# Performance work log

Hardware: AMD Instinct MI355X
Metric: run time of the kernel (lower is better)

The kernel has to match this reference:

```python
import jax, jax.numpy as jnp
import numpy as np

N = 50000          # nodes
E = 600000         # edges
D_IN = 256         # input_feat_dim
H1 = 128           # hidden_dim1
H2 = 64            # hidden_dim2
DK = 64            # trs_depth (total key/value depth)
HEADS = 2


def setup_inputs() -> dict:
    key = jax.random.key(0)
    ks = jax.random.split(key, 12)
    inp = {
        "ns_emb": jax.random.normal(ks[0], (N, D_IN), dtype=jnp.float32),
        "edge_rows": jax.random.randint(ks[1], (E,), 0, N, dtype=jnp.int32),
        "edge_cols": jax.random.randint(ks[2], (E,), 0, N, dtype=jnp.int32),
        "edge_vals": jax.random.uniform(ks[3], (E,), dtype=jnp.float32),
        "condition": jax.random.normal(ks[4], (1, 128, H1), dtype=jnp.float32),
        # GCN linear weights (bias=False), stored [in, out]
        "W_hidden": jax.random.normal(ks[5], (D_IN, H1), dtype=jnp.float32) / np.sqrt(D_IN),
        "W_mu": jax.random.normal(ks[6], (H1, H2), dtype=jnp.float32) / np.sqrt(H1),
        "W_var": jax.random.normal(ks[7], (H1, H2), dtype=jnp.float32) / np.sqrt(H1),
        # MultiHeadAttention (bias-free) projections
        "Wq": jax.random.normal(ks[8], (H1, DK), dtype=jnp.float32) / np.sqrt(H1),
        "Wk": jax.random.normal(ks[9], (H1, DK), dtype=jnp.float32) / np.sqrt(H1),
        "Wv": jax.random.normal(ks[10], (H1, DK), dtype=jnp.float32) / np.sqrt(H1),
        "Wo": jax.random.normal(ks[11], (DK, H1), dtype=jnp.float32) / np.sqrt(DK),
    }
    return inp


def _spmm(rows, cols, vals, x):
    # sparse [N,N] @ x  via gather + segment-sum over COO edges
    gathered = vals[:, None] * x[cols]            # [E, d]
    return jax.ops.segment_sum(gathered, rows, num_segments=N)


def _gcn(x, W, rows, cols, vals):
    # dropout is identity in eval mode
    support = jax.nn.leaky_relu(x @ W)            # [N, out]
    out = _spmm(rows, cols, vals, support)        # [N, out]
    return jax.nn.leaky_relu(out)


def _mha(q, kv, Wq, Wk, Wv, Wo):
    # MoEL-style MultiHeadAttention, bias-free, no mask/dropout
    B, Lq, _ = q.shape
    Lk = kv.shape[1]
    dk = DK // HEADS
    Q = (q @ Wq).reshape(B, Lq, HEADS, dk).transpose(0, 2, 1, 3) * (dk ** -0.5)
    K = (kv @ Wk).reshape(B, Lk, HEADS, dk).transpose(0, 2, 1, 3)
    V = (kv @ Wv).reshape(B, Lk, HEADS, dk).transpose(0, 2, 1, 3)
    logits = jnp.einsum("bhqd,bhkd->bhqk", Q, K)
    w = jax.nn.softmax(logits, axis=-1)
    ctx = jnp.einsum("bhqk,bhkd->bhqd", w, V)
    ctx = ctx.transpose(0, 2, 1, 3).reshape(B, Lq, DK)
    return ctx @ Wo, w


def reference(ns_emb, edge_rows, edge_cols, edge_vals, condition,
              W_hidden, W_mu, W_var, Wq, Wk, Wv, Wo):
    hidden = _gcn(ns_emb, W_hidden, edge_rows, edge_cols, edge_vals)   # [N, H1]
    attended, _ = _mha(hidden[None], condition, Wq, Wk, Wv, Wo)        # [1, N, H1]
    h = attended[0]
    mu = _gcn(h, W_mu, edge_rows, edge_cols, edge_vals)                # [N, H2]
    var = _gcn(h, W_var, edge_rows, edge_cols, edge_vals)              # [N, H2]
    return mu, var
```

## Files before the change

### kernel.cpp

```cpp
#include <hip/hip_runtime.h>
#include <hip/hip_bf16.h>
#include <cstdint>


typedef __attribute__((ext_vector_type(8))) short short8;
typedef __attribute__((ext_vector_type(4))) float f32x4;
typedef __attribute__((ext_vector_type(4))) unsigned short ushort4_t;

__device__ __forceinline__ unsigned short f2bf(float f) {
    unsigned int u = __builtin_bit_cast(unsigned int, f);
    u += 0x7fffu + ((u >> 16) & 1u);
    return (unsigned short)(u >> 16);
}
__device__ __forceinline__ float bf2f(unsigned short v) {
    return __builtin_bit_cast(float, (unsigned int)v << 16);
}


__global__ void hist_kernel(const int* __restrict__ rows, int* __restrict__ cnt, int E) {
    int i = blockIdx.x * blockDim.x + threadIdx.x;
    if (i < E) atomicAdd(&cnt[rows[i]], 1);
}

__global__ void scan1_kernel(const int* __restrict__ cnt, int* __restrict__ excl,
                             int* __restrict__ bsum, int N) {
    __shared__ int sh[256];
    int t = threadIdx.x;
    int i = blockIdx.x * 256 + t;
    int v = (i < N) ? cnt[i] : 0;
    sh[t] = v;
    __syncthreads();
    for (int off = 1; off < 256; off <<= 1) {
        int x = (t >= off) ? sh[t - off] : 0;
        __syncthreads();
        sh[t] += x;
        __syncthreads();
    }
    if (i < N) excl[i] = sh[t] - v;
    if (t == 255) bsum[blockIdx.x] = sh[255];
}

__global__ void scan2_kernel(int* __restrict__ bsum, int nb) {
    __shared__ int sh[256];
    int t = threadIdx.x;
    int v = (t < nb) ? bsum[t] : 0;
    sh[t] = v;
    __syncthreads();
    for (int off = 1; off < 256; off <<= 1) {
        int x = (t >= off) ? sh[t - off] : 0;
        __syncthreads();
        sh[t] += x;
        __syncthreads();
    }
    if (t < nb) bsum[t] = sh[t] - v;
}

__global__ void scan3_kernel(const int* __restrict__ excl, const int* __restrict__ bsum,
                             int* __restrict__ row_start, int* __restrict__ cursor,
                             int N, int E) {
    int i = blockIdx.x * 256 + threadIdx.x;
    if (i < N) {
        int v = excl[i] + bsum[i >> 8];
        row_start[i] = v;
        cursor[i] = v;
    }
    if (i == 0) row_start[N] = E;
}

__global__ void scatter_kernel(const int* __restrict__ rows, const int* __restrict__ colsIn,
                               const float* __restrict__ valsIn, int* __restrict__ cursor,
                               int2* __restrict__ pack, int E) {
    int i = blockIdx.x * blockDim.x + threadIdx.x;
    if (i < E) {
        int r = rows[i];
        int p = atomicAdd(&cursor[r], 1);
        pack[p] = make_int2(colsIn[i], __float_as_int(valsIn[i]));
    }
}


__global__ __launch_bounds__(256) void prep_weights(
    const float* __restrict__ Wh, const float* __restrict__ Wq,
    const float* __restrict__ Wo, const float* __restrict__ Wmu,
    const float* __restrict__ Wvar,
    unsigned short* __restrict__ WhT, unsigned short* __restrict__ WqT,
    unsigned short* __restrict__ WoT, unsigned short* __restrict__ WmuT,
    unsigned short* __restrict__ WvarT)
{
    int idx = blockIdx.x * 256 + threadIdx.x;
    if (idx < 32768) {
        int n = idx & 127, k = idx >> 7;
        WhT[n * 256 + k] = f2bf(Wh[k * 128 + n]);
    } else if (idx < 40960) {
        int i = idx - 32768, n = i & 63, k = i >> 6;
        WqT[n * 128 + k] = f2bf(Wq[k * 64 + n]);
    } else if (idx < 49152) {
        int i = idx - 40960, n = i & 127, k = i >> 7;
        WoT[n * 64 + k] = f2bf(Wo[k * 128 + n]);
    } else if (idx < 57344) {
        int i = idx - 49152, n = i & 63, k = i >> 6;
        WmuT[n * 128 + k] = f2bf(Wmu[k * 64 + n]);
    } else if (idx < 65536) {
        int i = idx - 57344, n = i & 63, k = i >> 6;
        WvarT[n * 128 + k] = f2bf(Wvar[k * 64 + n]);
    }
}


__global__ __launch_bounds__(128) void kv_kernel(
    const float* __restrict__ cond, const float* __restrict__ Wk,
    const float* __restrict__ Wv, unsigned short* __restrict__ Ktt,
    unsigned short* __restrict__ Vt)
{
    int j = blockIdx.x;
    int t = threadIdx.x;
    __shared__ float c[128];
    c[t] = cond[j * 128 + t];
    __syncthreads();
    const float* W = (t < 64) ? Wk : Wv;
    int col = t & 63;
    float acc = 0.f;
#pragma unroll 8
    for (int k = 0; k < 128; ++k) acc = fmaf(c[k], W[k * 64 + col], acc);
    int h = col >> 5, d = col & 31;
    if (t < 64) Ktt[((size_t)h * 128 + j) * 32 + d] = f2bf(acc * 0.17677669529663687f);
    else        Vt[((size_t)h * 32 + d) * 128 + j] = f2bf(acc);
}


__global__ __launch_bounds__(256) void gcn1_gemm(
    const float* __restrict__ A, const unsigned short* __restrict__ BT,
    unsigned short* __restrict__ C, int M)
{
    __shared__ unsigned short As[128][72];
    __shared__ unsigned short Bs[128][72];

    const int tid = threadIdx.x;
    const int lane = tid & 63, wave = tid >> 6;
    const int wm = wave & 1, wn = wave >> 1;
    const int quad = lane >> 4, l16 = lane & 15;
    const int r0 = blockIdx.x * 128;

    f32x4 acc[4][4];
#pragma unroll
    for (int mt = 0; mt < 4; ++mt)
#pragma unroll
        for (int nt = 0; nt < 4; ++nt)
#pragma unroll
            for (int r = 0; r < 4; ++r) acc[mt][nt][r] = 0.f;

    for (int kc = 0; kc < 256; kc += 64) {
#pragma unroll
        for (int i = 0; i < 8; ++i) {
            int f = tid + 256 * i;
            int row = f >> 4, kq = (f & 15) << 2;
            int gr = r0 + row;
            if (gr >= M) gr = M - 1;
            float4 v = *reinterpret_cast<const float4*>(&A[(size_t)gr * 256 + kc + kq]);
            ushort4_t pv;
            pv[0] = f2bf(v.x); pv[1] = f2bf(v.y); pv[2] = f2bf(v.z); pv[3] = f2bf(v.w);
            *reinterpret_cast<ushort4_t*>(&As[row][kq]) = pv;
        }
#pragma unroll
        for (int i = 0; i < 4; ++i) {
            int f = tid + 256 * i;
            int n = f >> 3, k8 = (f & 7) << 3;
            *reinterpret_cast<short8*>(&Bs[n][k8]) =
                *reinterpret_cast<const short8*>(&BT[(size_t)n * 256 + kc + k8]);
        }
        __syncthreads();

#pragma unroll
        for (int ks = 0; ks < 2; ++ks) {
            const int koff = ks * 32 + quad * 8;
            short8 a[4], b[4];
#pragma unroll
            for (int mt = 0; mt < 4; ++mt)
                a[mt] = *reinterpret_cast<const short8*>(&As[wm * 64 + mt * 16 + l16][koff]);
#pragma unroll
            for (int nt = 0; nt < 4; ++nt)
                b[nt] = *reinterpret_cast<const short8*>(&Bs[wn * 64 + nt * 16 + l16][koff]);
#pragma unroll
            for (int mt = 0; mt < 4; ++mt)
#pragma unroll
                for (int nt = 0; nt < 4; ++nt)
                    acc[mt][nt] = __builtin_amdgcn_mfma_f32_16x16x32_bf16(
                        a[mt], b[nt], acc[mt][nt], 0, 0, 0);
        }
        __syncthreads();
    }

#pragma unroll
    for (int mt = 0; mt < 4; ++mt)
#pragma unroll
        for (int nt = 0; nt < 4; ++nt) {
            int gc = wn * 64 + nt * 16 + l16;
#pragma unroll
            for (int r = 0; r < 4; ++r) {
                int gr = r0 + wm * 64 + mt * 16 + quad * 4 + r;
                if (gr < M) {
                    float v = acc[mt][nt][r];
                    v = v > 0.f ? v : 0.01f * v;
                    C[(size_t)gr * 128 + gc] = f2bf(v);
                }
            }
        }
}


__global__ __launch_bounds__(256) void attn_muvar_kernel(
    const unsigned short* __restrict__ hidden,
    const unsigned short* __restrict__ WqT,
    const unsigned short* __restrict__ Ktt,
    const unsigned short* __restrict__ Vt,
    const unsigned short* __restrict__ WoT,
    const unsigned short* __restrict__ WmuT,
    const unsigned short* __restrict__ WvarT,
    unsigned short* __restrict__ muvar,
    int M)
{
    __shared__ unsigned short Ap[128 * 136];
    __shared__ unsigned short Bp[10240];
    __shared__ unsigned short Cp[128 * 72];
    __shared__ float redm[2][128];
    __shared__ float reds[2][128];

    const int tid = threadIdx.x;
    const int lane = tid & 63, wave = tid >> 6;
    const int wm = wave & 1, wn = wave >> 1;
    const int quad = lane >> 4, l16 = lane & 15;
    const int r0 = blockIdx.x * 128;

#pragma unroll
    for (int i = 0; i < 8; ++i) {
        int f = tid + 256 * i;
        int row = f >> 4, k8 = (f & 15) << 3;
        int gr = r0 + row;
        if (gr >= M) gr = M - 1;
        *reinterpret_cast<short8*>(&Ap[row * 136 + k8]) =
            *reinterpret_cast<const short8*>(&hidden[(size_t)gr * 128 + k8]);
    }
#pragma unroll
    for (int i = 0; i < 4; ++i) {
        int f = tid + 256 * i;
        int n = f >> 4, k8 = (f & 15) << 3;
        *reinterpret_cast<short8*>(&Bp[n * 136 + k8]) =
            *reinterpret_cast<const short8*>(&WqT[(size_t)n * 128 + k8]);
    }
    __syncthreads();

    {
        f32x4 accq[4][2];
#pragma unroll
        for (int mt = 0; mt < 4; ++mt)
#pragma unroll
            for (int nt = 0; nt < 2; ++nt)
#pragma unroll
                for (int r = 0; r < 4; ++r) accq[mt][nt][r] = 0.f;
#pragma unroll
        for (int ks = 0; ks < 4; ++ks) {
            const int koff = ks * 32 + quad * 8;
            short8 a[4], b[2];
#pragma unroll
            for (int mt = 0; mt < 4; ++mt)
                a[mt] = *reinterpret_cast<const short8*>(&Ap[(wm * 64 + mt * 16 + l16) * 136 + koff]);
#pragma unroll
            for (int nt = 0; nt < 2; ++nt)
                b[nt] = *reinterpret_cast<const short8*>(&Bp[(wn * 32 + nt * 16 + l16) * 136 + koff]);
#pragma unroll
            for (int mt = 0; mt < 4; ++mt)
#pragma unroll
                for (int nt = 0; nt < 2; ++nt)
                    accq[mt][nt] = __builtin_amdgcn_mfma_f32_16x16x32_bf16(
                        a[mt], b[nt], accq[mt][nt], 0, 0, 0);
        }
#pragma unroll
        for (int mt = 0; mt < 4; ++mt)
#pragma unroll
            for (int nt = 0; nt < 2; ++nt) {
                int col = wn * 32 + nt * 16 + l16;
#pragma unroll
                for (int r = 0; r < 4; ++r) {
                    int row = wm * 64 + mt * 16 + quad * 4 + r;
                    Cp[row * 72 + col] = f2bf(accq[mt][nt][r]);
                }
            }
    }
    __syncthreads();

    for (int h = 0; h < 2; ++h) {
#pragma unroll
        for (int i = 0; i < 2; ++i) {
            int f = tid + 256 * i;
            int key = f >> 2, d8 = (f & 3) << 3;
            *reinterpret_cast<short8*>(&Bp[key * 40 + d8]) =
                *reinterpret_cast<const short8*>(&Ktt[((size_t)h * 128 + key) * 32 + d8]);
        }
#pragma unroll
        for (int i = 0; i < 2; ++i) {
            int f = tid + 256 * i;
            int d = f >> 4, k8 = (f & 15) << 3;
            *reinterpret_cast<short8*>(&Bp[5120 + d * 136 + k8]) =
                *reinterpret_cast<const short8*>(&Vt[((size_t)h * 32 + d) * 128 + k8]);
        }
        __syncthreads();

        f32x4 accl[4][4];
        {
            short8 a[4], b[4];
#pragma unroll
            for (int mt = 0; mt < 4; ++mt)
                a[mt] = *reinterpret_cast<const short8*>(&Cp[(wm * 64 + mt * 16 + l16) * 72 + h * 32 + quad * 8]);
#pragma unroll
            for (int nt = 0; nt < 4; ++nt)
                b[nt] = *reinterpret_cast<const short8*>(&Bp[(wn * 64 + nt * 16 + l16) * 40 + quad * 8]);
#pragma unroll
            for (int mt = 0; mt < 4; ++mt)
#pragma unroll
                for (int nt = 0; nt < 4; ++nt) {
                    f32x4 z; z[0] = 0.f; z[1] = 0.f; z[2] = 0.f; z[3] = 0.f;
                    accl[mt][nt] = __builtin_amdgcn_mfma_f32_16x16x32_bf16(a[mt], b[nt], z, 0, 0, 0);
                }
        }

#pragma unroll
        for (int mt = 0; mt < 4; ++mt)
#pragma unroll
            for (int r = 0; r < 4; ++r) {
                float mx = fmaxf(fmaxf(accl[mt][0][r], accl[mt][1][r]),
                                 fmaxf(accl[mt][2][r], accl[mt][3][r]));
#pragma unroll
                for (int off = 1; off < 16; off <<= 1)
                    mx = fmaxf(mx, __shfl_xor(mx, off, 64));
                if (l16 == 0) redm[wn][wm * 64 + mt * 16 + quad * 4 + r] = mx;
            }
        __syncthreads();
#pragma unroll
        for (int mt = 0; mt < 4; ++mt)
#pragma unroll
            for (int r = 0; r < 4; ++r) {
                int lr = wm * 64 + mt * 16 + quad * 4 + r;
                float fm = fmaxf(redm[0][lr], redm[1][lr]);
                float s = 0.f;
#pragma unroll
                for (int nt = 0; nt < 4; ++nt) {
                    float e = __expf(accl[mt][nt][r] - fm);
                    accl[mt][nt][r] = e;
                    s += e;
                }
#pragma unroll
                for (int off = 1; off < 16; off <<= 1)
                    s += __shfl_xor(s, off, 64);
                if (l16 == 0) reds[wn][lr] = s;
            }
        __syncthreads();
#pragma unroll
        for (int mt = 0; mt < 4; ++mt)
#pragma unroll
            for (int r = 0; r < 4; ++r) {
                int lr = wm * 64 + mt * 16 + quad * 4 + r;
                float inv = 1.0f / (reds[0][lr] + reds[1][lr]);
#pragma unroll
                for (int nt = 0; nt < 4; ++nt)
                    Ap[lr * 136 + wn * 64 + nt * 16 + l16] = f2bf(accl[mt][nt][r] * inv);
            }
        __syncthreads();

        {
            f32x4 accc[4];
#pragma unroll
            for (int mt = 0; mt < 4; ++mt)
#pragma unroll
                for (int r = 0; r < 4; ++r) accc[mt][r] = 0.f;
#pragma unroll
            for (int ks = 0; ks < 4; ++ks) {
                const int koff = ks * 32 + quad * 8;
                short8 a[4];
#pragma unroll
                for (int mt = 0; mt < 4; ++mt)
                    a[mt] = *reinterpret_cast<const short8*>(&Ap[(wm * 64 + mt * 16 + l16) * 136 + koff]);
                short8 bb = *reinterpret_cast<const short8*>(&Bp[5120 + (wn * 16 + l16) * 136 + koff]);
#pragma unroll
                for (int mt = 0; mt < 4; ++mt)
                    accc[mt] = __builtin_amdgcn_mfma_f32_16x16x32_bf16(a[mt], bb, accc[mt], 0, 0, 0);
            }
#pragma unroll
            for (int mt = 0; mt < 4; ++mt)
#pragma unroll
                for (int r = 0; r < 4; ++r) {
                    int row = wm * 64 + mt * 16 + quad * 4 + r;
                    Cp[row * 72 + h * 32 + wn * 16 + l16] = f2bf(accc[mt][r]);
                }
        }
        __syncthreads();
    }

#pragma unroll
    for (int i = 0; i < 4; ++i) {
        int f = tid + 256 * i;
        int n = f >> 3, k8 = (f & 7) << 3;
        *reinterpret_cast<short8*>(&Bp[n * 72 + k8]) =
            *reinterpret_cast<const short8*>(&WoT[(size_t)n * 64 + k8]);
    }
    __syncthreads();
    {
        f32x4 acca[4][4];
#pragma unroll
        for (int mt = 0; mt < 4; ++mt)
#pragma unroll
            for (int nt = 0; nt < 4; ++nt)
#pragma unroll
                for (int r = 0; r < 4; ++r) acca[mt][nt][r] = 0.f;
#pragma unroll
        for (int ks = 0; ks < 2; ++ks) {
            const int koff = ks * 32 + quad * 8;
            short8 a[4], b[4];
#pragma unroll
            for (int mt = 0; mt < 4; ++mt)
                a[mt] = *reinterpret_cast<const short8*>(&Cp[(wm * 64 + mt * 16 + l16) * 72 + koff]);
#pragma unroll
            for (int nt = 0; nt < 4; ++nt)
                b[nt] = *reinterpret_cast<const short8*>(&Bp[(wn * 64 + nt * 16 + l16) * 72 + koff]);
#pragma unroll
            for (int mt = 0; mt < 4; ++mt)
#pragma unroll
                for (int nt = 0; nt < 4; ++nt)
                    acca[mt][nt] = __builtin_amdgcn_mfma_f32_16x16x32_bf16(
                        a[mt], b[nt], acca[mt][nt], 0, 0, 0);
        }
#pragma unroll
        for (int mt = 0; mt < 4; ++mt)
#pragma unroll
            for (int nt = 0; nt < 4; ++nt) {
                int col = wn * 64 + nt * 16 + l16;
#pragma unroll
                for (int r = 0; r < 4; ++r) {
                    int row = wm * 64 + mt * 16 + quad * 4 + r;
                    Ap[row * 136 + col] = f2bf(acca[mt][nt][r]);
                }
            }
    }
    __syncthreads();

    for (int half = 0; half < 2; ++half) {
        const unsigned short* WT = half ? WvarT : WmuT;
#pragma unroll
        for (int i = 0; i < 4; ++i) {
            int f = tid + 256 * i;
            int n = f >> 4, k8 = (f & 15) << 3;
            *reinterpret_cast<short8*>(&Bp[n * 136 + k8]) =
                *reinterpret_cast<const short8*>(&WT[(size_t)n * 128 + k8]);
        }
        __syncthreads();
        f32x4 accm[4][2];
#pragma unroll
        for (int mt = 0; mt < 4; ++mt)
#pragma unroll
            for (int nt = 0; nt < 2; ++nt)
#pragma unroll
                for (int r = 0; r < 4; ++r) accm[mt][nt][r] = 0.f;
#pragma unroll
        for (int ks = 0; ks < 4; ++ks) {
            const int koff = ks * 32 + quad * 8;
            short8 a[4], b[2];
#pragma unroll
            for (int mt = 0; mt < 4; ++mt)
                a[mt] = *reinterpret_cast<const short8*>(&Ap[(wm * 64 + mt * 16 + l16) * 136 + koff]);
#pragma unroll
            for (int nt = 0; nt < 2; ++nt)
                b[nt] = *reinterpret_cast<const short8*>(&Bp[(wn * 32 + nt * 16 + l16) * 136 + koff]);
#pragma unroll
            for (int mt = 0; mt < 4; ++mt)
#pragma unroll
                for (int nt = 0; nt < 2; ++nt)
                    accm[mt][nt] = __builtin_amdgcn_mfma_f32_16x16x32_bf16(
                        a[mt], b[nt], accm[mt][nt], 0, 0, 0);
        }
#pragma unroll
        for (int mt = 0; mt < 4; ++mt)
#pragma unroll
            for (int nt = 0; nt < 2; ++nt) {
                int gc = half * 64 + wn * 32 + nt * 16 + l16;
#pragma unroll
                for (int r = 0; r < 4; ++r) {
                    int gr = r0 + wm * 64 + mt * 16 + quad * 4 + r;
                    if (gr < M) {
                        float v = accm[mt][nt][r];
                        v = v > 0.f ? v : 0.01f * v;
                        muvar[(size_t)gr * 128 + gc] = f2bf(v);
                    }
                }
            }
        __syncthreads();
    }
}


template<bool SPLIT, typename OT>
__global__ __launch_bounds__(256) void spmm_kernel(
    const int* __restrict__ row_start, const int2* __restrict__ pack,
    const unsigned short* __restrict__ X,
    OT* __restrict__ out0, OT* __restrict__ out1, int N)
{
    const int wave = threadIdx.x >> 6, lane = threadIdx.x & 63;
    int r = blockIdx.x * 4 + wave;
    if (r >= N) return;
    int s = __builtin_amdgcn_readfirstlane(row_start[r]);
    int e = __builtin_amdgcn_readfirstlane(row_start[r + 1]);
    const int fo = lane * 2;

    float ax0 = 0.f, ay0 = 0.f, ax1 = 0.f, ay1 = 0.f;
    float ax2 = 0.f, ay2 = 0.f, ax3 = 0.f, ay3 = 0.f;
    int i = s;
    for (; i + 4 <= e; i += 4) {
        int2 p0 = pack[i], p1 = pack[i + 1], p2 = pack[i + 2], p3 = pack[i + 3];
        unsigned int x0 = *reinterpret_cast<const unsigned int*>(&X[(size_t)p0.x * 128 + fo]);
        unsigned int x1 = *reinterpret_cast<const unsigned int*>(&X[(size_t)p1.x * 128 + fo]);
        unsigned int x2 = *reinterpret_cast<const unsigned int*>(&X[(size_t)p2.x * 128 + fo]);
        unsigned int x3 = *reinterpret_cast<const unsigned int*>(&X[(size_t)p3.x * 128 + fo]);
        float v0 = __int_as_float(p0.y), v1 = __int_as_float(p1.y);
        float v2 = __int_as_float(p2.y), v3 = __int_as_float(p3.y);
        ax0 = fmaf(v0, bf2f((unsigned short)x0), ax0);
        ay0 = fmaf(v0, bf2f((unsigned short)(x0 >> 16)), ay0);
        ax1 = fmaf(v1, bf2f((unsigned short)x1), ax1);
        ay1 = fmaf(v1, bf2f((unsigned short)(x1 >> 16)), ay1);
        ax2 = fmaf(v2, bf2f((unsigned short)x2), ax2);
        ay2 = fmaf(v2, bf2f((unsigned short)(x2 >> 16)), ay2);
        ax3 = fmaf(v3, bf2f((unsigned short)x3), ax3);
        ay3 = fmaf(v3, bf2f((unsigned short)(x3 >> 16)), ay3);
    }
    for (; i < e; ++i) {
        int2 p0 = pack[i];
        unsigned int x0 = *reinterpret_cast<const unsigned int*>(&X[(size_t)p0.x * 128 + fo]);
        float v0 = __int_as_float(p0.y);
        ax0 = fmaf(v0, bf2f((unsigned short)x0), ax0);
        ay0 = fmaf(v0, bf2f((unsigned short)(x0 >> 16)), ay0);
    }
    float ox = (ax0 + ax1) + (ax2 + ax3);
    float oy = (ay0 + ay1) + (ay2 + ay3);
    ox = ox > 0.f ? ox : 0.01f * ox;
    oy = oy > 0.f ? oy : 0.01f * oy;

    if constexpr (!SPLIT) {
        unsigned int w = (unsigned int)f2bf(ox) | ((unsigned int)f2bf(oy) << 16);
        *reinterpret_cast<unsigned int*>(&out0[(size_t)r * 128 + fo]) = w;
    } else {
        if (lane < 32) {
            float2 w = make_float2(ox, oy);
            *reinterpret_cast<float2*>(&out0[(size_t)r * 64 + fo]) = w;
        } else {
            float2 w = make_float2(ox, oy);
            *reinterpret_cast<float2*>(&out1[(size_t)r * 64 + (fo - 64)]) = w;
        }
    }
}


extern "C" void kernel_launch(void* const* d_in, const int* in_sizes, int n_in,
                              void* d_out, int out_size, void* d_ws, size_t ws_size,
                              hipStream_t stream)
{
    const float* ns_emb   = (const float*)d_in[0];
    const int*   erows    = (const int*)d_in[1];
    const int*   ecols    = (const int*)d_in[2];
    const float* evals    = (const float*)d_in[3];
    const float* cond     = (const float*)d_in[4];
    const float* W_hidden = (const float*)d_in[5];
    const float* W_mu     = (const float*)d_in[6];
    const float* W_var    = (const float*)d_in[7];
    const float* Wq       = (const float*)d_in[8];
    const float* Wk       = (const float*)d_in[9];
    const float* Wv       = (const float*)d_in[10];
    const float* Wo       = (const float*)d_in[11];

    const int N = in_sizes[0] / 256;
    const int E = in_sizes[1];

    typedef unsigned short bf16;
    uint8_t* p = (uint8_t*)d_ws;
    auto alloc = [&](size_t bytes) {
        uint8_t* r = p;
        p += (bytes + 255) & ~(size_t)255;
        return r;
    };
    bf16* support1 = (bf16*)alloc(sizeof(bf16) * (size_t)N * 128);
    bf16* hidden   = (bf16*)alloc(sizeof(bf16) * (size_t)N * 128);
    bf16* muvarb   = (bf16*)alloc(sizeof(bf16) * (size_t)N * 128);
    bf16* Ktt      = (bf16*)alloc(sizeof(bf16) * 2 * 128 * 32);
    bf16* Vt       = (bf16*)alloc(sizeof(bf16) * 2 * 32 * 128);
    bf16* WhT      = (bf16*)alloc(sizeof(bf16) * 128 * 256);
    bf16* WqT      = (bf16*)alloc(sizeof(bf16) * 64 * 128);
    bf16* WoT      = (bf16*)alloc(sizeof(bf16) * 128 * 64);
    bf16* WmuT     = (bf16*)alloc(sizeof(bf16) * 64 * 128);
    bf16* WvarT    = (bf16*)alloc(sizeof(bf16) * 64 * 128);
    int*  cnt      = (int*)alloc(sizeof(int) * N);
    int*  excl     = (int*)alloc(sizeof(int) * N);
    int*  bsum     = (int*)alloc(sizeof(int) * 256);
    int*  row_start= (int*)alloc(sizeof(int) * (N + 1));
    int*  cursor   = (int*)alloc(sizeof(int) * N);
    int2* pack     = (int2*)alloc(sizeof(int2) * E);

    hipMemsetAsync(cnt, 0, sizeof(int) * N, stream);
    hist_kernel<<<(E + 255) / 256, 256, 0, stream>>>(erows, cnt, E);
    int nb = (N + 255) / 256;
    scan1_kernel<<<nb, 256, 0, stream>>>(cnt, excl, bsum, N);
    scan2_kernel<<<1, 256, 0, stream>>>(bsum, nb);
    scan3_kernel<<<nb, 256, 0, stream>>>(excl, bsum, row_start, cursor, N, E);
    scatter_kernel<<<(E + 255) / 256, 256, 0, stream>>>(erows, ecols, evals, cursor, pack, E);

    prep_weights<<<256, 256, 0, stream>>>(W_hidden, Wq, Wo, W_mu, W_var,
                                          WhT, WqT, WoT, WmuT, WvarT);
    kv_kernel<<<128, 128, 0, stream>>>(cond, Wk, Wv, Ktt, Vt);

    const int mb = (N + 127) / 128;

    gcn1_gemm<<<mb, 256, 0, stream>>>(ns_emb, WhT, support1, N);
    spmm_kernel<false, bf16><<<(N + 3) / 4, 256, 0, stream>>>(
        row_start, pack, support1, hidden, nullptr, N);

    attn_muvar_kernel<<<mb, 256, 0, stream>>>(hidden, WqT, Ktt, Vt, WoT,
                                              WmuT, WvarT, muvarb, N);

    float* out = (float*)d_out;
    spmm_kernel<true, float><<<(N + 3) / 4, 256, 0, stream>>>(
        row_start, pack, muvarb, out, out + (size_t)N * 64, N);
}
```

Baseline: 276.1 us.

## Process two rows per wave in SpMM and merge small setup kernels

The SpMM kernel now has each wavefront handle two CSR rows at once, interleaving their gathers to raise memory-level parallelism and halve the number of waves. The scan2 and scan3 kernels are merged: every block redundantly scans the block sums. The weight-prep and K/V projection kernels are fused into one launch. Together these cut launch overhead and are meant to hide gather latency, at the cost of divergent row-length handling and more registers per wave.

```diff
diff --git a/kernel.cpp b/kernel.cpp
--- a/kernel.cpp
+++ b/kernel.cpp
@@ -40,7 +40,9 @@
     if (t == 255) bsum[blockIdx.x] = sh[255];
 }
 
-__global__ void scan2_kernel(int* __restrict__ bsum, int nb) {
+__global__ void scan23_kernel(const int* __restrict__ excl, const int* __restrict__ bsum,
+                              int* __restrict__ row_start, int* __restrict__ cursor,
+                              int nb, int N, int E) {
     __shared__ int sh[256];
     int t = threadIdx.x;
     int v = (t < nb) ? bsum[t] : 0;
@@ -52,17 +54,12 @@
         sh[t] += x;
         __syncthreads();
     }
-    if (t < nb) bsum[t] = sh[t] - v;
-}
-
-__global__ void scan3_kernel(const int* __restrict__ excl, const int* __restrict__ bsum,
-                             int* __restrict__ row_start, int* __restrict__ cursor,
-                             int N, int E) {
-    int i = blockIdx.x * 256 + threadIdx.x;
+    int boff = (blockIdx.x > 0) ? sh[blockIdx.x - 1] : 0;
+    int i = blockIdx.x * 256 + t;
     if (i < N) {
-        int v = excl[i] + bsum[i >> 8];
-        row_start[i] = v;
-        cursor[i] = v;
+        int w = excl[i] + boff;
+        row_start[i] = w;
+        cursor[i] = w;
     }
     if (i == 0) row_start[N] = E;
 }
@@ -79,52 +76,51 @@
 }
 
 
-__global__ __launch_bounds__(256) void prep_weights(
+__global__ __launch_bounds__(256) void prep_kv_kernel(
     const float* __restrict__ Wh, const float* __restrict__ Wq,
     const float* __restrict__ Wo, const float* __restrict__ Wmu,
-    const float* __restrict__ Wvar,
+    const float* __restrict__ Wvar, const float* __restrict__ cond,
+    const float* __restrict__ Wk, const float* __restrict__ Wv,
     unsigned short* __restrict__ WhT, unsigned short* __restrict__ WqT,
     unsigned short* __restrict__ WoT, unsigned short* __restrict__ WmuT,
-    unsigned short* __restrict__ WvarT)
-{
-    int idx = blockIdx.x * 256 + threadIdx.x;
-    if (idx < 32768) {
-        int n = idx & 127, k = idx >> 7;
-        WhT[n * 256 + k] = f2bf(Wh[k * 128 + n]);
-    } else if (idx < 40960) {
-        int i = idx - 32768, n = i & 63, k = i >> 6;
-        WqT[n * 128 + k] = f2bf(Wq[k * 64 + n]);
-    } else if (idx < 49152) {
-        int i = idx - 40960, n = i & 127, k = i >> 7;
-        WoT[n * 64 + k] = f2bf(Wo[k * 128 + n]);
-    } else if (idx < 57344) {
-        int i = idx - 49152, n = i & 63, k = i >> 6;
-        WmuT[n * 128 + k] = f2bf(Wmu[k * 64 + n]);
-    } else if (idx < 65536) {
-        int i = idx - 57344, n = i & 63, k = i >> 6;
-        WvarT[n * 128 + k] = f2bf(Wvar[k * 64 + n]);
-    }
-}
-
-
-__global__ __launch_bounds__(128) void kv_kernel(
-    const float* __restrict__ cond, const float* __restrict__ Wk,
-    const float* __restrict__ Wv, unsigned short* __restrict__ Ktt,
+    unsigned short* __restrict__ WvarT, unsigned short* __restrict__ Ktt,
     unsigned short* __restrict__ Vt)
 {
-    int j = blockIdx.x;
-    int t = threadIdx.x;
-    __shared__ float c[128];
-    c[t] = cond[j * 128 + t];
-    __syncthreads();
-    const float* W = (t < 64) ? Wk : Wv;
-    int col = t & 63;
-    float acc = 0.f;
+    const int t = threadIdx.x;
+    if (blockIdx.x < 256) {
+        int idx = blockIdx.x * 256 + t;
+        if (idx < 32768) {
+            int n = idx & 127, k = idx >> 7;
+            WhT[n * 256 + k] = f2bf(Wh[k * 128 + n]);
+        } else if (idx < 40960) {
+            int i = idx - 32768, n = i & 63, k = i >> 6;
+            WqT[n * 128 + k] = f2bf(Wq[k * 64 + n]);
+        } else if (idx < 49152) {
+            int i = idx - 40960, n = i & 127, k = i >> 7;
+            WoT[n * 64 + k] = f2bf(Wo[k * 128 + n]);
+        } else if (idx < 57344) {
+            int i = idx - 49152, n = i & 63, k = i >> 6;
+            WmuT[n * 128 + k] = f2bf(Wmu[k * 64 + n]);
+        } else if (idx < 65536) {
+            int i = idx - 57344, n = i & 63, k = i >> 6;
+            WvarT[n * 128 + k] = f2bf(Wvar[k * 64 + n]);
+        }
+    } else {
+        int b2 = blockIdx.x - 256;
+        __shared__ float c[2][128];
+        c[t >> 7][t & 127] = cond[b2 * 256 + t];
+        __syncthreads();
+        int j = b2 * 2 + (t >> 7);
+        int tl = t & 127;
+        const float* W = (tl < 64) ? Wk : Wv;
+        int col = tl & 63;
+        float acc = 0.f;
 #pragma unroll 8
-    for (int k = 0; k < 128; ++k) acc = fmaf(c[k], W[k * 64 + col], acc);
-    int h = col >> 5, d = col & 31;
-    if (t < 64) Ktt[((size_t)h * 128 + j) * 32 + d] = f2bf(acc * 0.17677669529663687f);
-    else        Vt[((size_t)h * 32 + d) * 128 + j] = f2bf(acc);
+        for (int k = 0; k < 128; ++k) acc = fmaf(c[t >> 7][k], W[k * 64 + col], acc);
+        int h = col >> 5, d = col & 31;
+        if (tl < 64) Ktt[((size_t)h * 128 + j) * 32 + d] = f2bf(acc * 0.17677669529663687f);
+        else         Vt[((size_t)h * 32 + d) * 128 + j] = f2bf(acc);
+    }
 }
 
 
@@ -503,54 +499,108 @@
     OT* __restrict__ out0, OT* __restrict__ out1, int N)
 {
     const int wave = threadIdx.x >> 6, lane = threadIdx.x & 63;
-    int r = blockIdx.x * 4 + wave;
-    if (r >= N) return;
-    int s = __builtin_amdgcn_readfirstlane(row_start[r]);
-    int e = __builtin_amdgcn_readfirstlane(row_start[r + 1]);
+    const int wid = blockIdx.x * 4 + wave;
+    const int ra = wid * 2, rb = ra + 1;
+    if (ra >= N) return;
+    const bool hasb = rb < N;
+    int sa = __builtin_amdgcn_readfirstlane(row_start[ra]);
+    int ea = __builtin_amdgcn_readfirstlane(row_start[ra + 1]);
+    int sb = hasb ? __builtin_amdgcn_readfirstlane(row_start[rb]) : 0;
+    int eb = hasb ? __builtin_amdgcn_readfirstlane(row_start[rb + 1]) : 0;
     const int fo = lane * 2;
 
-    float ax0 = 0.f, ay0 = 0.f, ax1 = 0.f, ay1 = 0.f;
-    float ax2 = 0.f, ay2 = 0.f, ax3 = 0.f, ay3 = 0.f;
-    int i = s;
-    for (; i + 4 <= e; i += 4) {
-        int2 p0 = pack[i], p1 = pack[i + 1], p2 = pack[i + 2], p3 = pack[i + 3];
-        unsigned int x0 = *reinterpret_cast<const unsigned int*>(&X[(size_t)p0.x * 128 + fo]);
-        unsigned int x1 = *reinterpret_cast<const unsigned int*>(&X[(size_t)p1.x * 128 + fo]);
-        unsigned int x2 = *reinterpret_cast<const unsigned int*>(&X[(size_t)p2.x * 128 + fo]);
-        unsigned int x3 = *reinterpret_cast<const unsigned int*>(&X[(size_t)p3.x * 128 + fo]);
-        float v0 = __int_as_float(p0.y), v1 = __int_as_float(p1.y);
-        float v2 = __int_as_float(p2.y), v3 = __int_as_float(p3.y);
-        ax0 = fmaf(v0, bf2f((unsigned short)x0), ax0);
-        ay0 = fmaf(v0, bf2f((unsigned short)(x0 >> 16)), ay0);
-        ax1 = fmaf(v1, bf2f((unsigned short)x1), ax1);
-        ay1 = fmaf(v1, bf2f((unsigned short)(x1 >> 16)), ay1);
-        ax2 = fmaf(v2, bf2f((unsigned short)x2), ax2);
-        ay2 = fmaf(v2, bf2f((unsigned short)(x2 >> 16)), ay2);
-        ax3 = fmaf(v3, bf2f((unsigned short)x3), ax3);
-        ay3 = fmaf(v3, bf2f((unsigned short)(x3 >> 16)), ay3);
-    }
-    for (; i < e; ++i) {
-        int2 p0 = pack[i];
-        unsigned int x0 = *reinterpret_cast<const unsigned int*>(&X[(size_t)p0.x * 128 + fo]);
-        float v0 = __int_as_float(p0.y);
-        ax0 = fmaf(v0, bf2f((unsigned short)x0), ax0);
-        ay0 = fmaf(v0, bf2f((unsigned short)(x0 >> 16)), ay0);
-    }
-    float ox = (ax0 + ax1) + (ax2 + ax3);
-    float oy = (ay0 + ay1) + (ay2 + ay3);
-    ox = ox > 0.f ? ox : 0.01f * ox;
-    oy = oy > 0.f ? oy : 0.01f * oy;
+    float aax[4] = {0.f, 0.f, 0.f, 0.f}, aay[4] = {0.f, 0.f, 0.f, 0.f};
+    float abx[4] = {0.f, 0.f, 0.f, 0.f}, aby[4] = {0.f, 0.f, 0.f, 0.f};
+    int ia = sa, ib = sb;
+
+    while ((ia + 4 <= ea) | (ib + 4 <= eb)) {
+        const bool da = ia + 4 <= ea, db = ib + 4 <= eb;
+        int2 pa[4], pb[4];
+        unsigned int xa[4], xb[4];
+        if (da) {
+#pragma unroll
+            for (int k = 0; k < 4; ++k) pa[k] = pack[ia + k];
+        }
+        if (db) {
+#pragma unroll
+            for (int k = 0; k < 4; ++k) pb[k] = pack[ib + k];
+        }
+        if (da) {
+#pragma unroll
+            for (int k = 0; k < 4; ++k)
+                xa[k] = *reinterpret_cast<const unsigned int*>(&X[(size_t)pa[k].x * 128 + fo]);
+        }
+        if (db) {
+#pragma unroll
+            for (int k = 0; k < 4; ++k)
+                xb[k] = *reinterpret_cast<const unsigned int*>(&X[(size_t)pb[k].x * 128 + fo]);
+        }
+        if (da) {
+#pragma unroll
+            for (int k = 0; k < 4; ++k) {
+                float v = __int_as_float(pa[k].y);
+                aax[k] = fmaf(v, bf2f((unsigned short)xa[k]), aax[k]);
+                aay[k] = fmaf(v, bf2f((unsigned short)(xa[k] >> 16)), aay[k]);
+            }
+            ia += 4;
+        }
+        if (db) {
+#pragma unroll
+            for (int k = 0; k < 4; ++k) {
+                float v = __int_as_float(pb[k].y);
+                abx[k] = fmaf(v, bf2f((unsigned short)xb[k]), abx[k]);
+                aby[k] = fmaf(v, bf2f((unsigned short)(xb[k] >> 16)), aby[k]);
+            }
+            ib += 4;
+        }
+    }
+    while ((ia < ea) | (ib < eb)) {
+        const bool ta = ia < ea, tb = ib < eb;
+        int2 pa, pb;
+        unsigned int xa, xb;
+        if (ta) pa = pack[ia];
+        if (tb) pb = pack[ib];
+        if (ta) xa = *reinterpret_cast<const unsigned int*>(&X[(size_t)pa.x * 128 + fo]);
+        if (tb) xb = *reinterpret_cast<const unsigned int*>(&X[(size_t)pb.x * 128 + fo]);
+        if (ta) {
+            float v = __int_as_float(pa.y);
+            aax[0] = fmaf(v, bf2f((unsigned short)xa), aax[0]);
+            aay[0] = fmaf(v, bf2f((unsigned short)(xa >> 16)), aay[0]);
+            ++ia;
+        }
+        if (tb) {
+            float v = __int_as_float(pb.y);
+            abx[0] = fmaf(v, bf2f((unsigned short)xb), abx[0]);
+            aby[0] = fmaf(v, bf2f((unsigned short)(xb >> 16)), aby[0]);
+            ++ib;
+        }
+    }
+
+    float oxa = (aax[0] + aax[1]) + (aax[2] + aax[3]);
+    float oya = (aay[0] + aay[1]) + (aay[2] + aay[3]);
+    oxa = oxa > 0.f ? oxa : 0.01f * oxa;
+    oya = oya > 0.f ? oya : 0.01f * oya;
+    float oxb = (abx[0] + abx[1]) + (abx[2] + abx[3]);
+    float oyb = (aby[0] + aby[1]) + (aby[2] + aby[3]);
+    oxb = oxb > 0.f ? oxb : 0.01f * oxb;
+    oyb = oyb > 0.f ? oyb : 0.01f * oyb;
 
     if constexpr (!SPLIT) {
-        unsigned int w = (unsigned int)f2bf(ox) | ((unsigned int)f2bf(oy) << 16);
-        *reinterpret_cast<unsigned int*>(&out0[(size_t)r * 128 + fo]) = w;
+        unsigned int wa = (unsigned int)f2bf(oxa) | ((unsigned int)f2bf(oya) << 16);
+        *reinterpret_cast<unsigned int*>(&out0[(size_t)ra * 128 + fo]) = wa;
+        if (hasb) {
+            unsigned int wb = (unsigned int)f2bf(oxb) | ((unsigned int)f2bf(oyb) << 16);
+            *reinterpret_cast<unsigned int*>(&out0[(size_t)rb * 128 + fo]) = wb;
+        }
     } else {
         if (lane < 32) {
-            float2 w = make_float2(ox, oy);
-            *reinterpret_cast<float2*>(&out0[(size_t)r * 64 + fo]) = w;
+            *reinterpret_cast<float2*>(&out0[(size_t)ra * 64 + fo]) = make_float2(oxa, oya);
+            if (hasb)
+                *reinterpret_cast<float2*>(&out0[(size_t)rb * 64 + fo]) = make_float2(oxb, oyb);
         } else {
-            float2 w = make_float2(ox, oy);
-            *reinterpret_cast<float2*>(&out1[(size_t)r * 64 + (fo - 64)]) = w;
+            *reinterpret_cast<float2*>(&out1[(size_t)ra * 64 + (fo - 64)]) = make_float2(oxa, oya);
+            if (hasb)
+                *reinterpret_cast<float2*>(&out1[(size_t)rb * 64 + (fo - 64)]) = make_float2(oxb, oyb);
         }
     }
 }
@@ -604,24 +654,24 @@
     hist_kernel<<<(E + 255) / 256, 256, 0, stream>>>(erows, cnt, E);
     int nb = (N + 255) / 256;
     scan1_kernel<<<nb, 256, 0, stream>>>(cnt, excl, bsum, N);
-    scan2_kernel<<<1, 256, 0, stream>>>(bsum, nb);
-    scan3_kernel<<<nb, 256, 0, stream>>>(excl, bsum, row_start, cursor, N, E);
+    scan23_kernel<<<nb, 256, 0, stream>>>(excl, bsum, row_start, cursor, nb, N, E);
     scatter_kernel<<<(E + 255) / 256, 256, 0, stream>>>(erows, ecols, evals, cursor, pack, E);
 
-    prep_weights<<<256, 256, 0, stream>>>(W_hidden, Wq, Wo, W_mu, W_var,
-                                          WhT, WqT, WoT, WmuT, WvarT);
-    kv_kernel<<<128, 128, 0, stream>>>(cond, Wk, Wv, Ktt, Vt);
+    prep_kv_kernel<<<320, 256, 0, stream>>>(W_hidden, Wq, Wo, W_mu, W_var,
+                                            cond, Wk, Wv,
+                                            WhT, WqT, WoT, WmuT, WvarT, Ktt, Vt);
 
     const int mb = (N + 127) / 128;
+    const int sblocks = ((N + 1) / 2 + 3) / 4;
 
     gcn1_gemm<<<mb, 256, 0, stream>>>(ns_emb, WhT, support1, N);
-    spmm_kernel<false, bf16><<<(N + 3) / 4, 256, 0, stream>>>(
+    spmm_kernel<false, bf16><<<sblocks, 256, 0, stream>>>(
         row_start, pack, support1, hidden, nullptr, N);
 
     attn_muvar_kernel<<<mb, 256, 0, stream>>>(hidden, WqT, Ktt, Vt, WoT,
                                               WmuT, WvarT, muvarb, N);
 
     float* out = (float*)d_out;
-    spmm_kernel<true, float><<<(N + 3) / 4, 256, 0, stream>>>(
+    spmm_kernel<true, float><<<sblocks, 256, 0, stream>>>(
         row_start, pack, muvarb, out, out + (size_t)N * 64, N);
 }
```

After: 289.4 us. 4.8% more time.

## Split SpMM rows across two waves and merge small setup kernels

Applied to the files above, without the earlier changes.

The SpMM kernel now gives each row two waves, each handling 64 features with one bf16 per lane, instead of one wave handling two features per lane. This doubles the waves in flight to hide gather latency, but every edge's pack entry is now loaded twice and each lane issues narrower 2-byte gathers and stores. Separately, scan2 and scan3 are fused by having every block redo the block-sum scan, and the weight-prep and K/V projection kernels are merged into one launch to cut launch count.

```diff
diff --git a/kernel.cpp b/kernel.cpp
--- a/kernel.cpp
+++ b/kernel.cpp
@@ -40,7 +40,9 @@
     if (t == 255) bsum[blockIdx.x] = sh[255];
 }
 
-__global__ void scan2_kernel(int* __restrict__ bsum, int nb) {
+__global__ void scan23_kernel(const int* __restrict__ excl, const int* __restrict__ bsum,
+                              int* __restrict__ row_start, int* __restrict__ cursor,
+                              int nb, int N, int E) {
     __shared__ int sh[256];
     int t = threadIdx.x;
     int v = (t < nb) ? bsum[t] : 0;
@@ -52,17 +54,12 @@
         sh[t] += x;
         __syncthreads();
     }
-    if (t < nb) bsum[t] = sh[t] - v;
-}
-
-__global__ void scan3_kernel(const int* __restrict__ excl, const int* __restrict__ bsum,
-                             int* __restrict__ row_start, int* __restrict__ cursor,
-                             int N, int E) {
-    int i = blockIdx.x * 256 + threadIdx.x;
+    int boff = (blockIdx.x > 0) ? sh[blockIdx.x - 1] : 0;
+    int i = blockIdx.x * 256 + t;
     if (i < N) {
-        int v = excl[i] + bsum[i >> 8];
-        row_start[i] = v;
-        cursor[i] = v;
+        int w = excl[i] + boff;
+        row_start[i] = w;
+        cursor[i] = w;
     }
     if (i == 0) row_start[N] = E;
 }
@@ -79,52 +76,51 @@
 }
 
 
-__global__ __launch_bounds__(256) void prep_weights(
+__global__ __launch_bounds__(256) void prep_kv_kernel(
     const float* __restrict__ Wh, const float* __restrict__ Wq,
     const float* __restrict__ Wo, const float* __restrict__ Wmu,
-    const float* __restrict__ Wvar,
+    const float* __restrict__ Wvar, const float* __restrict__ cond,
+    const float* __restrict__ Wk, const float* __restrict__ Wv,
     unsigned short* __restrict__ WhT, unsigned short* __restrict__ WqT,
     unsigned short* __restrict__ WoT, unsigned short* __restrict__ WmuT,
-    unsigned short* __restrict__ WvarT)
-{
-    int idx = blockIdx.x * 256 + threadIdx.x;
-    if (idx < 32768) {
-        int n = idx & 127, k = idx >> 7;
-        WhT[n * 256 + k] = f2bf(Wh[k * 128 + n]);
-    } else if (idx < 40960) {
-        int i = idx - 32768, n = i & 63, k = i >> 6;
-        WqT[n * 128 + k] = f2bf(Wq[k * 64 + n]);
-    } else if (idx < 49152) {
-        int i = idx - 40960, n = i & 127, k = i >> 7;
-        WoT[n * 64 + k] = f2bf(Wo[k * 128 + n]);
-    } else if (idx < 57344) {
-        int i = idx - 49152, n = i & 63, k = i >> 6;
-        WmuT[n * 128 + k] = f2bf(Wmu[k * 64 + n]);
-    } else if (idx < 65536) {
-        int i = idx - 57344, n = i & 63, k = i >> 6;
-        WvarT[n * 128 + k] = f2bf(Wvar[k * 64 + n]);
-    }
-}
-
-
-__global__ __launch_bounds__(128) void kv_kernel(
-    const float* __restrict__ cond, const float* __restrict__ Wk,
-    const float* __restrict__ Wv, unsigned short* __restrict__ Ktt,
+    unsigned short* __restrict__ WvarT, unsigned short* __restrict__ Ktt,
     unsigned short* __restrict__ Vt)
 {
-    int j = blockIdx.x;
-    int t = threadIdx.x;
-    __shared__ float c[128];
-    c[t] = cond[j * 128 + t];
-    __syncthreads();
-    const float* W = (t < 64) ? Wk : Wv;
-    int col = t & 63;
-    float acc = 0.f;
+    const int t = threadIdx.x;
+    if (blockIdx.x < 256) {
+        int idx = blockIdx.x * 256 + t;
+        if (idx < 32768) {
+            int n = idx & 127, k = idx >> 7;
+            WhT[n * 256 + k] = f2bf(Wh[k * 128 + n]);
+        } else if (idx < 40960) {
+            int i = idx - 32768, n = i & 63, k = i >> 6;
+            WqT[n * 128 + k] = f2bf(Wq[k * 64 + n]);
+        } else if (idx < 49152) {
+            int i = idx - 40960, n = i & 127, k = i >> 7;
+            WoT[n * 64 + k] = f2bf(Wo[k * 128 + n]);
+        } else if (idx < 57344) {
+            int i = idx - 49152, n = i & 63, k = i >> 6;
+            WmuT[n * 128 + k] = f2bf(Wmu[k * 64 + n]);
+        } else if (idx < 65536) {
+            int i = idx - 57344, n = i & 63, k = i >> 6;
+            WvarT[n * 128 + k] = f2bf(Wvar[k * 64 + n]);
+        }
+    } else {
+        int b2 = blockIdx.x - 256;
+        __shared__ float c[2][128];
+        c[t >> 7][t & 127] = cond[b2 * 256 + t];
+        __syncthreads();
+        int j = b2 * 2 + (t >> 7);
+        int tl = t & 127;
+        const float* W = (tl < 64) ? Wk : Wv;
+        int col = tl & 63;
+        float acc = 0.f;
 #pragma unroll 8
-    for (int k = 0; k < 128; ++k) acc = fmaf(c[k], W[k * 64 + col], acc);
-    int h = col >> 5, d = col & 31;
-    if (t < 64) Ktt[((size_t)h * 128 + j) * 32 + d] = f2bf(acc * 0.17677669529663687f);
-    else        Vt[((size_t)h * 32 + d) * 128 + j] = f2bf(acc);
+        for (int k = 0; k < 128; ++k) acc = fmaf(c[t >> 7][k], W[k * 64 + col], acc);
+        int h = col >> 5, d = col & 31;
+        if (tl < 64) Ktt[((size_t)h * 128 + j) * 32 + d] = f2bf(acc * 0.17677669529663687f);
+        else         Vt[((size_t)h * 32 + d) * 128 + j] = f2bf(acc);
+    }
 }
 
 
@@ -503,55 +499,40 @@
     OT* __restrict__ out0, OT* __restrict__ out1, int N)
 {
     const int wave = threadIdx.x >> 6, lane = threadIdx.x & 63;
-    int r = blockIdx.x * 4 + wave;
+    const int gwave = blockIdx.x * 4 + wave;
+    const int r = gwave >> 1;
+    const int half = gwave & 1;
     if (r >= N) return;
     int s = __builtin_amdgcn_readfirstlane(row_start[r]);
     int e = __builtin_amdgcn_readfirstlane(row_start[r + 1]);
-    const int fo = lane * 2;
-
-    float ax0 = 0.f, ay0 = 0.f, ax1 = 0.f, ay1 = 0.f;
-    float ax2 = 0.f, ay2 = 0.f, ax3 = 0.f, ay3 = 0.f;
+    const int fo = half * 64 + lane;
+
+    float a0 = 0.f, a1 = 0.f, a2 = 0.f, a3 = 0.f;
     int i = s;
     for (; i + 4 <= e; i += 4) {
         int2 p0 = pack[i], p1 = pack[i + 1], p2 = pack[i + 2], p3 = pack[i + 3];
-        unsigned int x0 = *reinterpret_cast<const unsigned int*>(&X[(size_t)p0.x * 128 + fo]);
-        unsigned int x1 = *reinterpret_cast<const unsigned int*>(&X[(size_t)p1.x * 128 + fo]);
-        unsigned int x2 = *reinterpret_cast<const unsigned int*>(&X[(size_t)p2.x * 128 + fo]);
-        unsigned int x3 = *reinterpret_cast<const unsigned int*>(&X[(size_t)p3.x * 128 + fo]);
-        float v0 = __int_as_float(p0.y), v1 = __int_as_float(p1.y);
-        float v2 = __int_as_float(p2.y), v3 = __int_as_float(p3.y);
-        ax0 = fmaf(v0, bf2f((unsigned short)x0), ax0);
-        ay0 = fmaf(v0, bf2f((unsigned short)(x0 >> 16)), ay0);
-        ax1 = fmaf(v1, bf2f((unsigned short)x1), ax1);
-        ay1 = fmaf(v1, bf2f((unsigned short)(x1 >> 16)), ay1);
-        ax2 = fmaf(v2, bf2f((unsigned short)x2), ax2);
-        ay2 = fmaf(v2, bf2f((unsigned short)(x2 >> 16)), ay2);
-        ax3 = fmaf(v3, bf2f((unsigned short)x3), ax3);
-        ay3 = fmaf(v3, bf2f((unsigned short)(x3 >> 16)), ay3);
+        unsigned short x0 = X[(size_t)p0.x * 128 + fo];
+        unsigned short x1 = X[(size_t)p1.x * 128 + fo];
+        unsigned short x2 = X[(size_t)p2.x * 128 + fo];
+        unsigned short x3 = X[(size_t)p3.x * 128 + fo];
+        a0 = fmaf(__int_as_float(p0.y), bf2f(x0), a0);
+        a1 = fmaf(__int_as_float(p1.y), bf2f(x1), a1);
+        a2 = fmaf(__int_as_float(p2.y), bf2f(x2), a2);
+        a3 = fmaf(__int_as_float(p3.y), bf2f(x3), a3);
     }
     for (; i < e; ++i) {
         int2 p0 = pack[i];
-        unsigned int x0 = *reinterpret_cast<const unsigned int*>(&X[(size_t)p0.x * 128 + fo]);
-        float v0 = __int_as_float(p0.y);
-        ax0 = fmaf(v0, bf2f((unsigned short)x0), ax0);
-        ay0 = fmaf(v0, bf2f((unsigned short)(x0 >> 16)), ay0);
-    }
-    float ox = (ax0 + ax1) + (ax2 + ax3);
-    float oy = (ay0 + ay1) + (ay2 + ay3);
-    ox = ox > 0.f ? ox : 0.01f * ox;
-    oy = oy > 0.f ? oy : 0.01f * oy;
+        unsigned short x0 = X[(size_t)p0.x * 128 + fo];
+        a0 = fmaf(__int_as_float(p0.y), bf2f(x0), a0);
+    }
+    float o = (a0 + a1) + (a2 + a3);
+    o = o > 0.f ? o : 0.01f * o;
 
     if constexpr (!SPLIT) {
-        unsigned int w = (unsigned int)f2bf(ox) | ((unsigned int)f2bf(oy) << 16);
-        *reinterpret_cast<unsigned int*>(&out0[(size_t)r * 128 + fo]) = w;
+        out0[(size_t)r * 128 + fo] = (OT)f2bf(o);
     } else {
-        if (lane < 32) {
-            float2 w = make_float2(ox, oy);
-            *reinterpret_cast<float2*>(&out0[(size_t)r * 64 + fo]) = w;
-        } else {
-            float2 w = make_float2(ox, oy);
-            *reinterpret_cast<float2*>(&out1[(size_t)r * 64 + (fo - 64)]) = w;
-        }
+        if (half == 0) out0[(size_t)r * 64 + lane] = o;
+        else           out1[(size_t)r * 64 + lane] = o;
     }
 }
 
@@ -604,24 +585,24 @@
     hist_kernel<<<(E + 255) / 256, 256, 0, stream>>>(erows, cnt, E);
     int nb = (N + 255) / 256;
     scan1_kernel<<<nb, 256, 0, stream>>>(cnt, excl, bsum, N);
-    scan2_kernel<<<1, 256, 0, stream>>>(bsum, nb);
-    scan3_kernel<<<nb, 256, 0, stream>>>(excl, bsum, row_start, cursor, N, E);
+    scan23_kernel<<<nb, 256, 0, stream>>>(excl, bsum, row_start, cursor, nb, N, E);
     scatter_kernel<<<(E + 255) / 256, 256, 0, stream>>>(erows, ecols, evals, cursor, pack, E);
 
-    prep_weights<<<256, 256, 0, stream>>>(W_hidden, Wq, Wo, W_mu, W_var,
-                                          WhT, WqT, WoT, WmuT, WvarT);
-    kv_kernel<<<128, 128, 0, stream>>>(cond, Wk, Wv, Ktt, Vt);
+    prep_kv_kernel<<<320, 256, 0, stream>>>(W_hidden, Wq, Wo, W_mu, W_var,
+                                            cond, Wk, Wv,
+                                            WhT, WqT, WoT, WmuT, WvarT, Ktt, Vt);
 
     const int mb = (N + 127) / 128;
+    const int sblocks = (2 * N + 3) / 4;
 
     gcn1_gemm<<<mb, 256, 0, stream>>>(ns_emb, WhT, support1, N);
-    spmm_kernel<false, bf16><<<(N + 3) / 4, 256, 0, stream>>>(
+    spmm_kernel<false, bf16><<<sblocks, 256, 0, stream>>>(
         row_start, pack, support1, hidden, nullptr, N);
 
     attn_muvar_kernel<<<mb, 256, 0, stream>>>(hidden, WqT, Ktt, Vt, WoT,
                                               WmuT, WvarT, muvarb, N);
 
     float* out = (float*)d_out;
-    spmm_kernel<true, float><<<(N + 3) / 4, 256, 0, stream>>>(
+    spmm_kernel<true, float><<<sblocks, 256, 0, stream>>>(
         row_start, pack, muvarb, out, out + (size_t)N * 64, N);
 }
```

Measured after the change: 300.5 us. +8.8%, slower.
